# Performance work log

Measured on AMD Instinct MI355X. Metric: run time of the kernel, lower is better.

## Reference

```python
import jax, jax.numpy as jnp
import numpy as np

N = 50000      # nodes
E = 800000     # edges (before self-loops)
H = 4          # attention heads
C = 32         # out_features per head
DIN = 128      # in_features (== H*C so residual path is active)
ED = 16        # edge_dim
NEG = 0.2      # LeakyReLU negative slope (GATConv default)
EPS = 1e-5     # LayerNorm eps


def setup_inputs() -> dict:
    key = jax.random.key(0)
    ks = jax.random.split(key, 12)
    s = 0.05
    return {
        "x": jax.random.normal(ks[0], (N, DIN), dtype=jnp.float32),
        "edge_index": jax.random.randint(ks[1], (2, E), 0, N, dtype=jnp.int64),
        "edge_attr": jax.random.normal(ks[2], (E, ED), dtype=jnp.float32),
        # edge_processor: Linear(ED, ED) + ReLU (dropout = identity at eval)
        "W_ep": jax.random.normal(ks[3], (ED, ED), dtype=jnp.float32) * s,
        "b_ep": jnp.zeros((ED,), dtype=jnp.float32),
        # GATConv params (lin / lin_edge are bias-free in PyG)
        "W_lin": jax.random.normal(ks[4], (DIN, H * C), dtype=jnp.float32) * s,
        "W_edge": jax.random.normal(ks[5], (ED, H * C), dtype=jnp.float32) * s,
        "att_src": jax.random.normal(ks[6], (H, C), dtype=jnp.float32) * s,
        "att_dst": jax.random.normal(ks[7], (H, C), dtype=jnp.float32) * s,
        "att_edge": jax.random.normal(ks[8], (H, C), dtype=jnp.float32) * s,
        "bias": jnp.zeros((H * C,), dtype=jnp.float32),
        # LayerNorm params
        "ln_g": jnp.ones((H * C,), dtype=jnp.float32),
        "ln_b": jnp.zeros((H * C,), dtype=jnp.float32),
    }


def reference(x, edge_index, edge_attr, W_ep, b_ep, W_lin, W_edge,
              att_src, att_dst, att_edge, bias, ln_g, ln_b):
    n = x.shape[0]
    src, dst = edge_index[0], edge_index[1]

    # edge_processor: Linear + ReLU
    ea = jax.nn.relu(edge_attr @ W_ep + b_ep)                       # [E, ED]

    # add self-loops (PyG GATConv default), loop edge_attr = mean of incoming
    ones = jnp.ones((ea.shape[0],), dtype=ea.dtype)
    deg = jax.ops.segment_sum(ones, dst, num_segments=n)            # [N]
    loop_attr = jax.ops.segment_sum(ea, dst, num_segments=n)
    loop_attr = loop_attr / jnp.maximum(deg, 1.0)[:, None]          # [N, ED]
    loop = jnp.arange(n, dtype=src.dtype)
    src2 = jnp.concatenate([src, loop])                             # [E+N]
    dst2 = jnp.concatenate([dst, loop])
    ea2 = jnp.concatenate([ea, loop_attr], axis=0)                  # [E+N, ED]

    # node / edge linear transforms
    h = (x @ W_lin).reshape(n, H, C)                                # [N, H, C]
    a_src = jnp.einsum('nhc,hc->nh', h, att_src)                    # [N, H]
    a_dst = jnp.einsum('nhc,hc->nh', h, att_dst)
    e = (ea2 @ W_edge).reshape(-1, H, C)                            # [E+N, H, C]
    a_e = jnp.einsum('ehc,hc->eh', e, att_edge)                     # [E+N, H]

    # per-edge attention logits + leaky relu
    alpha = a_src[src2] + a_dst[dst2] + a_e                         # [E+N, H]
    alpha = jnp.where(alpha >= 0, alpha, NEG * alpha)

    # segment softmax over incoming edges of each dst node
    m = jax.ops.segment_max(alpha, dst2, num_segments=n)            # [N, H]
    ex = jnp.exp(alpha - m[dst2])
    denom = jax.ops.segment_sum(ex, dst2, num_segments=n)           # [N, H]
    w = ex / denom[dst2]                                            # [E+N, H]

    # scatter-aggregate messages
    msg = h[src2] * w[:, :, None]                                   # [E+N, H, C]
    out = jax.ops.segment_sum(msg, dst2, num_segments=n)            # [N, H, C]
    out = out.reshape(n, H * C) + bias

    # residual (DIN == H*C) + LayerNorm
    out = out + x
    mu = jnp.mean(out, axis=-1, keepdims=True)
    var = jnp.var(out, axis=-1, keepdims=True)
    out = (out - mu) * jax.lax.rsqrt(var + EPS) * ln_g + ln_b
    return out
```

## Files before the change

### kernel.cpp

```cpp
#include <hip/hip_runtime.h>
#include <hip/hip_fp16.h>
#include <math.h>

#define NN   50000
#define EE   800000
#define HH   4
#define CC   32
#define DINN 128
#define ED   16
#define NEGS 0.2f
#define LNEPS 1e-5f
#define SCAN_NB ((NN + 255) / 256)

struct __align__(16) Rec {
    float4  expa;
    __half2 ae01;
    __half2 ae23;
    int     src;
    int     pad;
};

struct __align__(8) Hp { __half2 a, b; };

__global__ __launch_bounds__(256, 2) void k_node(
        const float* __restrict__ x, const float* __restrict__ W_lin,
        const float* __restrict__ att_src, const float* __restrict__ att_dst,
        __half* __restrict__ hb, float* __restrict__ a_src, float* __restrict__ a_dst) {
    __shared__ float Wl[DINN * DINN];
    __shared__ float xr[32 * DINN];
    int t = threadIdx.x;

    {
        const float4* Wg = (const float4*)W_lin;
        float4* Ws = (float4*)Wl;
        #pragma unroll
        for (int i = 0; i < 16; ++i) Ws[t + 256 * i] = Wg[t + 256 * i];
    }
    int row0 = blockIdx.x * 32;
    {
        const float4* xg = (const float4*)x;
        float4* xs = (float4*)xr;
        #pragma unroll
        for (int i = 0; i < 4; ++i) {
            int idx = t + 256 * i;
            int row = row0 + (idx >> 5);
            float4 v = make_float4(0.f, 0.f, 0.f, 0.f);
            if (row < NN) v = xg[(long)row * 32 + (idx & 31)];
            xs[idx] = v;
        }
    }
    __syncthreads();

    int cg = t & 31, rg = t >> 5;
    int j0 = cg * 4;
    float acc[4][4] = {};
    #pragma unroll 4
    for (int k = 0; k < DINN; ++k) {
        float4 w = *(const float4*)&Wl[k * DINN + j0];
        #pragma unroll
        for (int i = 0; i < 4; ++i) {
            float xv = xr[(rg * 4 + i) * DINN + k];
            acc[i][0] = fmaf(xv, w.x, acc[i][0]);
            acc[i][1] = fmaf(xv, w.y, acc[i][1]);
            acc[i][2] = fmaf(xv, w.z, acc[i][2]);
            acc[i][3] = fmaf(xv, w.w, acc[i][3]);
        }
    }

    int head = cg >> 3, c0 = (cg & 7) * 4;
    float4 as4 = *(const float4*)&att_src[head * CC + c0];
    float4 ad4 = *(const float4*)&att_dst[head * CC + c0];
    #pragma unroll
    for (int i = 0; i < 4; ++i) {
        int row = row0 + rg * 4 + i;
        if (row < NN) {
            Hp p;
            p.a = __floats2half2_rn(acc[i][0], acc[i][1]);
            p.b = __floats2half2_rn(acc[i][2], acc[i][3]);
            *(Hp*)&hb[(long)row * DINN + j0] = p;
        }
        float ps = acc[i][0] * as4.x + acc[i][1] * as4.y + acc[i][2] * as4.z + acc[i][3] * as4.w;
        float pd = acc[i][0] * ad4.x + acc[i][1] * ad4.y + acc[i][2] * ad4.z + acc[i][3] * ad4.w;
        #pragma unroll
        for (int mask = 1; mask < 8; mask <<= 1) {
            ps += __shfl_xor(ps, mask);
            pd += __shfl_xor(pd, mask);
        }
        if ((cg & 7) == 0 && row < NN) {
            a_src[row * 4 + head] = ps;
            a_dst[row * 4 + head] = pd;
        }
    }
}

__global__ __launch_bounds__(256) void k_count(const int* __restrict__ ei,
                                               int* __restrict__ cnt,
                                               int* __restrict__ rank) {
    int e = blockIdx.x * 256 + threadIdx.x;
    if (e < EE) rank[e] = atomicAdd(cnt + ei[EE + e], 1);
}

__global__ __launch_bounds__(256) void k_scanA(const int* __restrict__ cnt,
                                               int* __restrict__ partial) {
    int t = threadIdx.x, b = blockIdx.x;
    int i = b * 256 + t;
    int v = (i < NN) ? cnt[i] : 0;
    #pragma unroll
    for (int d = 1; d < 64; d <<= 1) v += __shfl_xor(v, d);
    __shared__ int wt[4];
    if ((t & 63) == 0) wt[t >> 6] = v;
    __syncthreads();
    if (t == 0) partial[b] = wt[0] + wt[1] + wt[2] + wt[3];
}

__global__ __launch_bounds__(256) void k_scanB(const int* __restrict__ partial,
                                               int* __restrict__ poff,
                                               int* __restrict__ row_start,
                                               const float* __restrict__ W_edge,
                                               const float* __restrict__ att_edge,
                                               float* __restrict__ v_edge) {
    int t = threadIdx.x;
    if (t < ED * HH) {
        int d = t >> 2, h = t & 3;
        float s = 0.f;
        for (int c = 0; c < CC; ++c)
            s += W_edge[d * (HH * CC) + h * CC + c] * att_edge[h * CC + c];
        v_edge[t] = s;
    }
    int lane = t & 63, w = t >> 6;
    int v = (t < SCAN_NB) ? partial[t] : 0;
    int sv = v;
    #pragma unroll
    for (int d = 1; d < 64; d <<= 1) {
        int o = __shfl_up(sv, d);
        if (lane >= d) sv += o;
    }
    __shared__ int wt[4];
    if (lane == 63) wt[w] = sv;
    __syncthreads();
    int base = 0;
    for (int j = 0; j < w; ++j) base += wt[j];
    if (t < SCAN_NB) poff[t] = base + sv - v;
    if (t == 255) row_start[NN] = wt[0] + wt[1] + wt[2] + wt[3];
}

__global__ __launch_bounds__(256) void k_scanC(const int* __restrict__ cnt,
                                               const int* __restrict__ poff,
                                               int* __restrict__ row_start) {
    int t = threadIdx.x, b = blockIdx.x;
    int i = b * 256 + t;
    int v = (i < NN) ? cnt[i] : 0;
    int lane = t & 63, w = t >> 6;
    int sv = v;
    #pragma unroll
    for (int d = 1; d < 64; d <<= 1) {
        int o = __shfl_up(sv, d);
        if (lane >= d) sv += o;
    }
    __shared__ int wt[4];
    if (lane == 63) wt[w] = sv;
    __syncthreads();
    int base = 0;
    for (int j = 0; j < w; ++j) base += wt[j];
    if (i < NN) row_start[i] = poff[b] + base + sv - v;
}

__global__ __launch_bounds__(256) void k_edge2(
        const int* __restrict__ ei, const float* __restrict__ edge_attr,
        const float* __restrict__ W_ep, const float* __restrict__ b_ep,
        const float* __restrict__ v_edge,
        const float* __restrict__ a_src, const float* __restrict__ a_dst,
        const int* __restrict__ row_start, const int* __restrict__ rank,
        Rec* __restrict__ rec) {
    __shared__ float Wl[ED * ED];
    __shared__ float bl[ED];
    __shared__ float vl[ED * 4];
    int t = threadIdx.x;
    if (t < ED * ED) Wl[t] = W_ep[t];
    if (t < ED) bl[t] = b_ep[t];
    if (t < ED * 4) vl[t] = v_edge[t];
    __syncthreads();

    int e = blockIdx.x * 256 + t;
    if (e >= EE) return;

    float a[ED];
    const float4* ap = (const float4*)(edge_attr + (long)e * ED);
    float4 a0 = ap[0], a1 = ap[1], a2 = ap[2], a3 = ap[3];
    a[0]=a0.x; a[1]=a0.y; a[2]=a0.z; a[3]=a0.w;
    a[4]=a1.x; a[5]=a1.y; a[6]=a1.z; a[7]=a1.w;
    a[8]=a2.x; a[9]=a2.y; a[10]=a2.z; a[11]=a2.w;
    a[12]=a3.x; a[13]=a3.y; a[14]=a3.z; a[15]=a3.w;

    float r[ED];
    #pragma unroll
    for (int j = 0; j < ED; ++j) r[j] = bl[j];
    #pragma unroll
    for (int d = 0; d < ED; ++d) {
        float av = a[d];
        #pragma unroll
        for (int j = 0; j < ED; ++j) r[j] = fmaf(av, Wl[d * ED + j], r[j]);
    }

    float ae0 = 0.f, ae1 = 0.f, ae2 = 0.f, ae3 = 0.f;
    #pragma unroll
    for (int d = 0; d < ED; ++d) {
        float rd = fmaxf(r[d], 0.f);
        ae0 = fmaf(rd, vl[d * 4 + 0], ae0);
        ae1 = fmaf(rd, vl[d * 4 + 1], ae1);
        ae2 = fmaf(rd, vl[d * 4 + 2], ae2);
        ae3 = fmaf(rd, vl[d * 4 + 3], ae3);
    }

    int src = ei[e];
    int dst = ei[EE + e];
    float4 s4 = *(const float4*)&a_src[src * 4];
    float4 d4 = *(const float4*)&a_dst[dst * 4];
    float v0 = s4.x + d4.x + ae0;
    float v1 = s4.y + d4.y + ae1;
    float v2 = s4.z + d4.z + ae2;
    float v3 = s4.w + d4.w + ae3;
    v0 = (v0 >= 0.f) ? v0 : NEGS * v0;
    v1 = (v1 >= 0.f) ? v1 : NEGS * v1;
    v2 = (v2 >= 0.f) ? v2 : NEGS * v2;
    v3 = (v3 >= 0.f) ? v3 : NEGS * v3;

    Rec rc;
    rc.expa = make_float4(__expf(v0), __expf(v1), __expf(v2), __expf(v3));
    rc.ae01 = __floats2half2_rn(ae0, ae1);
    rc.ae23 = __floats2half2_rn(ae2, ae3);
    rc.src  = src;
    rc.pad  = 0;
    rec[row_start[dst] + rank[e]] = rc;
}

__global__ __launch_bounds__(256) void k_aggregate(
        const float* __restrict__ x, const __half2* __restrict__ hb,
        const float* __restrict__ a_src, const float* __restrict__ a_dst,
        const int* __restrict__ row_start, const Rec* __restrict__ rec,
        const float* __restrict__ bias, const float* __restrict__ ln_g,
        const float* __restrict__ ln_b, float* __restrict__ out) {
    int t = threadIdx.x;
    int wave = t >> 6, lane = t & 63;
    int n = blockIdx.x * 4 + wave;
    if (n >= NN) return;

    int start = row_start[n];
    int deg   = row_start[n + 1] - start;

    bool h1 = (lane & 32) != 0;
    bool h0 = (lane & 16) != 0;
    float accx = 0.f, accy = 0.f, s_own = 0.f, aes_own = 0.f;

    auto doEdge = [&](const Rec& r, __half2 hv) {
        float4 e4 = r.expa;
        float2 ef = h1 ? make_float2(e4.z, e4.w) : make_float2(e4.x, e4.y);
        float w = h0 ? ef.y : ef.x;
        float2 aef = __half22float2(h1 ? r.ae23 : r.ae01);
        aes_own += h0 ? aef.y : aef.x;
        s_own += w;
        float2 hf = __half22float2(hv);
        accx = fmaf(w, hf.x, accx);
        accy = fmaf(w, hf.y, accy);
    };

    const Rec* rp = rec + start;
    int k = 0;
    for (; k + 4 <= deg; k += 4) {
        Rec r0 = rp[k], r1 = rp[k + 1], r2 = rp[k + 2], r3 = rp[k + 3];
        __half2 v0 = hb[(long)r0.src * 64 + lane];
        __half2 v1 = hb[(long)r1.src * 64 + lane];
        __half2 v2 = hb[(long)r2.src * 64 + lane];
        __half2 v3 = hb[(long)r3.src * 64 + lane];
        doEdge(r0, v0); doEdge(r1, v1); doEdge(r2, v2); doEdge(r3, v3);
    }
    for (; k < deg; ++k) {
        Rec r = rp[k];
        doEdge(r, hb[(long)r.src * 64 + lane]);
    }

    int head = lane >> 4;
    float inv_deg = 1.0f / fmaxf((float)deg, 1.0f);
    float v = a_src[n * 4 + head] + a_dst[n * 4 + head] + aes_own * inv_deg;
    v = (v >= 0.f) ? v : NEGS * v;
    float w0 = __expf(v);
    s_own += w0;
    float2 hn = __half22float2(hb[(long)n * 64 + lane]);
    accx = fmaf(w0, hn.x, accx);
    accy = fmaf(w0, hn.y, accy);
    float is = 1.0f / s_own;
    accx *= is; accy *= is;

    int c0 = lane * 2;
    float2 b2 = *(const float2*)&bias[c0];
    float2 x2 = *(const float2*)&x[(long)n * DINN + c0];
    float oa = accx + b2.x + x2.x;
    float ob = accy + b2.y + x2.y;
    float sum = oa + ob, sumsq = oa * oa + ob * ob;
    #pragma unroll
    for (int d2 = 1; d2 < 64; d2 <<= 1) {
        sum   += __shfl_xor(sum, d2);
        sumsq += __shfl_xor(sumsq, d2);
    }
    float mu  = sum * (1.0f / DINN);
    float var = sumsq * (1.0f / DINN) - mu * mu;
    float rs  = rsqrtf(var + LNEPS);
    float2 g2  = *(const float2*)&ln_g[c0];
    float2 lb2 = *(const float2*)&ln_b[c0];
    float2 o2;
    o2.x = (oa - mu) * rs * g2.x + lb2.x;
    o2.y = (ob - mu) * rs * g2.y + lb2.y;
    *(float2*)&out[(long)n * DINN + c0] = o2;
}

extern "C" void kernel_launch(void* const* d_in, const int* in_sizes, int n_in,
                              void* d_out, int out_size, void* d_ws, size_t ws_size,
                              hipStream_t stream) {
    const float* x         = (const float*)d_in[0];
    const int*   ei        = (const int*)d_in[1];
    const float* edge_attr = (const float*)d_in[2];
    const float* W_ep      = (const float*)d_in[3];
    const float* b_ep      = (const float*)d_in[4];
    const float* W_lin     = (const float*)d_in[5];
    const float* W_edge    = (const float*)d_in[6];
    const float* att_src   = (const float*)d_in[7];
    const float* att_dst   = (const float*)d_in[8];
    const float* att_edge  = (const float*)d_in[9];
    const float* bias      = (const float*)d_in[10];
    const float* ln_g      = (const float*)d_in[11];
    const float* ln_b      = (const float*)d_in[12];
    float* out = (float*)d_out;

    char* ws = (char*)d_ws;
    size_t o = 0;
    auto take = [&](size_t bytes) -> char* {
        char* p = ws + o;
        o = (o + bytes + 255) & ~(size_t)255;
        return p;
    };
    __half* hbuf      = (__half*)take((size_t)NN * DINN * 2);
    float*  a_src     = (float*)take((size_t)NN * 4 * 4);
    float*  a_dst     = (float*)take((size_t)NN * 4 * 4);
    float*  v_edge    = (float*)take((size_t)ED * 4 * 4);
    int*    cnt       = (int*)  take((size_t)NN * 4);
    int*    row_start = (int*)  take((size_t)(NN + 1) * 4);
    int*    rank      = (int*)  take((size_t)EE * 4);
    int*    partial   = (int*)  take((size_t)SCAN_NB * 4);
    int*    poff      = (int*)  take((size_t)SCAN_NB * 4);
    Rec*    rec       = (Rec*)  take((size_t)EE * sizeof(Rec));

    hipMemsetAsync(cnt, 0, (size_t)NN * 4, stream);

    k_node<<<(NN + 31) / 32, 256, 0, stream>>>(x, W_lin, att_src, att_dst,
                                               hbuf, a_src, a_dst);
    k_count<<<(EE + 255) / 256, 256, 0, stream>>>(ei, cnt, rank);
    k_scanA<<<SCAN_NB, 256, 0, stream>>>(cnt, partial);
    k_scanB<<<1, 256, 0, stream>>>(partial, poff, row_start, W_edge, att_edge, v_edge);
    k_scanC<<<SCAN_NB, 256, 0, stream>>>(cnt, poff, row_start);
    k_edge2<<<(EE + 255) / 256, 256, 0, stream>>>(ei, edge_attr, W_ep, b_ep, v_edge,
                                                  a_src, a_dst, row_start, rank, rec);
    k_aggregate<<<(NN + 3) / 4, 256, 0, stream>>>(x, (const __half2*)hbuf,
                                                  a_src, a_dst, row_start, rec,
                                                  bias, ln_g, ln_b, out);
}
```

Measured before the change: 305.5 us.

## Split edge records into packed half2 weights plus separate CSR source array

The per-edge record changes from a 32-byte struct (fp32 exp weights, half attention terms, src) to a 16-byte packed array of half2 (exp, edge logit) per head plus a separate int source array. The aggregation kernel reads only its head's 4-byte word and batches 8 edges per iteration so more gathers are in flight. The node projection kernel no longer stages W_lin in LDS: it reads it from global/cache, uses 64-row tiles with a padded x tile and an 8-column register block per thread, and raises occupancy to 3 blocks per SM. Storing exp weights in half precision adds rounding and overflow risk for large logits.

```diff
diff --git a/kernel.cpp b/kernel.cpp
--- a/kernel.cpp
+++ b/kernel.cpp
@@ -12,81 +12,84 @@
 #define LNEPS 1e-5f
 #define SCAN_NB ((NN + 255) / 256)
 
-struct __align__(16) Rec {
-    float4  expa;
-    __half2 ae01;
-    __half2 ae23;
-    int     src;
-    int     pad;
-};
-
-struct __align__(8) Hp { __half2 a, b; };
-
-__global__ __launch_bounds__(256, 2) void k_node(
+struct __align__(16) Hp4 { __half2 a, b, c, d; };
+
+__global__ __launch_bounds__(256, 3) void k_node(
         const float* __restrict__ x, const float* __restrict__ W_lin,
         const float* __restrict__ att_src, const float* __restrict__ att_dst,
         __half* __restrict__ hb, float* __restrict__ a_src, float* __restrict__ a_dst) {
-    __shared__ float Wl[DINN * DINN];
-    __shared__ float xr[32 * DINN];
+    __shared__ float xr[64 * 132];
     int t = threadIdx.x;
-
-    {
-        const float4* Wg = (const float4*)W_lin;
-        float4* Ws = (float4*)Wl;
-        #pragma unroll
-        for (int i = 0; i < 16; ++i) Ws[t + 256 * i] = Wg[t + 256 * i];
-    }
-    int row0 = blockIdx.x * 32;
-    {
-        const float4* xg = (const float4*)x;
-        float4* xs = (float4*)xr;
+    int row0 = blockIdx.x * 64;
+
+    #pragma unroll
+    for (int i = 0; i < 8; ++i) {
+        int idx = t + 256 * i;
+        int r = idx >> 5, kq = idx & 31;
+        int row = row0 + r;
+        float4 v = make_float4(0.f, 0.f, 0.f, 0.f);
+        if (row < NN) v = ((const float4*)x)[(long)row * 32 + kq];
+        *(float4*)&xr[r * 132 + kq * 4] = v;
+    }
+    __syncthreads();
+
+    int colg = t & 15, rowg = t >> 4;
+    int c0 = colg * 8;
+    const float* Wp = W_lin + c0;
+    float acc[4][8] = {};
+
+    #pragma unroll 2
+    for (int k = 0; k < DINN; k += 2) {
+        float4 wa0 = *(const float4*)&Wp[(long)k * DINN];
+        float4 wb0 = *(const float4*)&Wp[(long)k * DINN + 4];
+        float4 wa1 = *(const float4*)&Wp[(long)(k + 1) * DINN];
+        float4 wb1 = *(const float4*)&Wp[(long)(k + 1) * DINN + 4];
         #pragma unroll
         for (int i = 0; i < 4; ++i) {
-            int idx = t + 256 * i;
-            int row = row0 + (idx >> 5);
-            float4 v = make_float4(0.f, 0.f, 0.f, 0.f);
-            if (row < NN) v = xg[(long)row * 32 + (idx & 31)];
-            xs[idx] = v;
-        }
-    }
-    __syncthreads();
-
-    int cg = t & 31, rg = t >> 5;
-    int j0 = cg * 4;
-    float acc[4][4] = {};
-    #pragma unroll 4
-    for (int k = 0; k < DINN; ++k) {
-        float4 w = *(const float4*)&Wl[k * DINN + j0];
-        #pragma unroll
-        for (int i = 0; i < 4; ++i) {
-            float xv = xr[(rg * 4 + i) * DINN + k];
-            acc[i][0] = fmaf(xv, w.x, acc[i][0]);
-            acc[i][1] = fmaf(xv, w.y, acc[i][1]);
-            acc[i][2] = fmaf(xv, w.z, acc[i][2]);
-            acc[i][3] = fmaf(xv, w.w, acc[i][3]);
-        }
-    }
-
-    int head = cg >> 3, c0 = (cg & 7) * 4;
-    float4 as4 = *(const float4*)&att_src[head * CC + c0];
-    float4 ad4 = *(const float4*)&att_dst[head * CC + c0];
+            float2 xv = *(const float2*)&xr[(rowg * 4 + i) * 132 + k];
+            acc[i][0] = fmaf(xv.x, wa0.x, acc[i][0]);
+            acc[i][1] = fmaf(xv.x, wa0.y, acc[i][1]);
+            acc[i][2] = fmaf(xv.x, wa0.z, acc[i][2]);
+            acc[i][3] = fmaf(xv.x, wa0.w, acc[i][3]);
+            acc[i][4] = fmaf(xv.x, wb0.x, acc[i][4]);
+            acc[i][5] = fmaf(xv.x, wb0.y, acc[i][5]);
+            acc[i][6] = fmaf(xv.x, wb0.z, acc[i][6]);
+            acc[i][7] = fmaf(xv.x, wb0.w, acc[i][7]);
+            acc[i][0] = fmaf(xv.y, wa1.x, acc[i][0]);
+            acc[i][1] = fmaf(xv.y, wa1.y, acc[i][1]);
+            acc[i][2] = fmaf(xv.y, wa1.z, acc[i][2]);
+            acc[i][3] = fmaf(xv.y, wa1.w, acc[i][3]);
+            acc[i][4] = fmaf(xv.y, wb1.x, acc[i][4]);
+            acc[i][5] = fmaf(xv.y, wb1.y, acc[i][5]);
+            acc[i][6] = fmaf(xv.y, wb1.z, acc[i][6]);
+            acc[i][7] = fmaf(xv.y, wb1.w, acc[i][7]);
+        }
+    }
+
+    int head = colg >> 2;
+    int cw = c0 & 31;
+    float4 as0 = *(const float4*)&att_src[head * CC + cw];
+    float4 as1 = *(const float4*)&att_src[head * CC + cw + 4];
+    float4 ad0 = *(const float4*)&att_dst[head * CC + cw];
+    float4 ad1 = *(const float4*)&att_dst[head * CC + cw + 4];
     #pragma unroll
     for (int i = 0; i < 4; ++i) {
-        int row = row0 + rg * 4 + i;
+        int row = row0 + rowg * 4 + i;
         if (row < NN) {
-            Hp p;
+            Hp4 p;
             p.a = __floats2half2_rn(acc[i][0], acc[i][1]);
             p.b = __floats2half2_rn(acc[i][2], acc[i][3]);
-            *(Hp*)&hb[(long)row * DINN + j0] = p;
-        }
-        float ps = acc[i][0] * as4.x + acc[i][1] * as4.y + acc[i][2] * as4.z + acc[i][3] * as4.w;
-        float pd = acc[i][0] * ad4.x + acc[i][1] * ad4.y + acc[i][2] * ad4.z + acc[i][3] * ad4.w;
-        #pragma unroll
-        for (int mask = 1; mask < 8; mask <<= 1) {
-            ps += __shfl_xor(ps, mask);
-            pd += __shfl_xor(pd, mask);
-        }
-        if ((cg & 7) == 0 && row < NN) {
+            p.c = __floats2half2_rn(acc[i][4], acc[i][5]);
+            p.d = __floats2half2_rn(acc[i][6], acc[i][7]);
+            *(Hp4*)&hb[(long)row * DINN + c0] = p;
+        }
+        float ps = acc[i][0]*as0.x + acc[i][1]*as0.y + acc[i][2]*as0.z + acc[i][3]*as0.w
+                 + acc[i][4]*as1.x + acc[i][5]*as1.y + acc[i][6]*as1.z + acc[i][7]*as1.w;
+        float pd = acc[i][0]*ad0.x + acc[i][1]*ad0.y + acc[i][2]*ad0.z + acc[i][3]*ad0.w
+                 + acc[i][4]*ad1.x + acc[i][5]*ad1.y + acc[i][6]*ad1.z + acc[i][7]*ad1.w;
+        ps += __shfl_xor(ps, 1); ps += __shfl_xor(ps, 2);
+        pd += __shfl_xor(pd, 1); pd += __shfl_xor(pd, 2);
+        if ((colg & 3) == 0 && row < NN) {
             a_src[row * 4 + head] = ps;
             a_dst[row * 4 + head] = pd;
         }
@@ -171,7 +174,7 @@
         const float* __restrict__ v_edge,
         const float* __restrict__ a_src, const float* __restrict__ a_dst,
         const int* __restrict__ row_start, const int* __restrict__ rank,
-        Rec* __restrict__ rec) {
+        uint4* __restrict__ pk, int* __restrict__ csr_src) {
     __shared__ float Wl[ED * ED];
     __shared__ float bl[ED];
     __shared__ float vl[ED * 4];
@@ -225,19 +228,21 @@
     v2 = (v2 >= 0.f) ? v2 : NEGS * v2;
     v3 = (v3 >= 0.f) ? v3 : NEGS * v3;
 
-    Rec rc;
-    rc.expa = make_float4(__expf(v0), __expf(v1), __expf(v2), __expf(v3));
-    rc.ae01 = __floats2half2_rn(ae0, ae1);
-    rc.ae23 = __floats2half2_rn(ae2, ae3);
-    rc.src  = src;
-    rc.pad  = 0;
-    rec[row_start[dst] + rank[e]] = rc;
+    __half2 p0 = __floats2half2_rn(__expf(v0), ae0);
+    __half2 p1 = __floats2half2_rn(__expf(v1), ae1);
+    __half2 p2 = __floats2half2_rn(__expf(v2), ae2);
+    __half2 p3 = __floats2half2_rn(__expf(v3), ae3);
+    int pos = row_start[dst] + rank[e];
+    pk[pos] = make_uint4(*(unsigned*)&p0, *(unsigned*)&p1,
+                         *(unsigned*)&p2, *(unsigned*)&p3);
+    csr_src[pos] = src;
 }
 
 __global__ __launch_bounds__(256) void k_aggregate(
         const float* __restrict__ x, const __half2* __restrict__ hb,
         const float* __restrict__ a_src, const float* __restrict__ a_dst,
-        const int* __restrict__ row_start, const Rec* __restrict__ rec,
+        const int* __restrict__ row_start,
+        const unsigned* __restrict__ pkh, const int* __restrict__ srcs,
         const float* __restrict__ bias, const float* __restrict__ ln_g,
         const float* __restrict__ ln_b, float* __restrict__ out) {
     int t = threadIdx.x;
@@ -247,39 +252,45 @@
 
     int start = row_start[n];
     int deg   = row_start[n + 1] - start;
-
-    bool h1 = (lane & 32) != 0;
-    bool h0 = (lane & 16) != 0;
+    int head  = lane >> 4;
+
     float accx = 0.f, accy = 0.f, s_own = 0.f, aes_own = 0.f;
-
-    auto doEdge = [&](const Rec& r, __half2 hv) {
-        float4 e4 = r.expa;
-        float2 ef = h1 ? make_float2(e4.z, e4.w) : make_float2(e4.x, e4.y);
-        float w = h0 ? ef.y : ef.x;
-        float2 aef = __half22float2(h1 ? r.ae23 : r.ae01);
-        aes_own += h0 ? aef.y : aef.x;
-        s_own += w;
+    const unsigned* pp = pkh + (size_t)start * 4 + head;
+    const int* sp = srcs + start;
+
+    int k = 0;
+    for (; k + 8 <= deg; k += 8) {
+        unsigned pv[8]; int sv[8];
+        #pragma unroll
+        for (int j = 0; j < 8; ++j) {
+            pv[j] = pp[(size_t)(k + j) * 4];
+            sv[j] = sp[k + j];
+        }
+        __half2 hv[8];
+        #pragma unroll
+        for (int j = 0; j < 8; ++j) hv[j] = hb[(long)sv[j] * 64 + lane];
+        #pragma unroll
+        for (int j = 0; j < 8; ++j) {
+            float2 wf = __half22float2(*(__half2*)&pv[j]);
+            s_own += wf.x;
+            aes_own += wf.y;
+            float2 hf = __half22float2(hv[j]);
+            accx = fmaf(wf.x, hf.x, accx);
+            accy = fmaf(wf.x, hf.y, accy);
+        }
+    }
+    for (; k < deg; ++k) {
+        unsigned p = pp[(size_t)k * 4];
+        int src = sp[k];
+        __half2 hv = hb[(long)src * 64 + lane];
+        float2 wf = __half22float2(*(__half2*)&p);
+        s_own += wf.x;
+        aes_own += wf.y;
         float2 hf = __half22float2(hv);
-        accx = fmaf(w, hf.x, accx);
-        accy = fmaf(w, hf.y, accy);
-    };
-
-    const Rec* rp = rec + start;
-    int k = 0;
-    for (; k + 4 <= deg; k += 4) {
-        Rec r0 = rp[k], r1 = rp[k + 1], r2 = rp[k + 2], r3 = rp[k + 3];
-        __half2 v0 = hb[(long)r0.src * 64 + lane];
-        __half2 v1 = hb[(long)r1.src * 64 + lane];
-        __half2 v2 = hb[(long)r2.src * 64 + lane];
-        __half2 v3 = hb[(long)r3.src * 64 + lane];
-        doEdge(r0, v0); doEdge(r1, v1); doEdge(r2, v2); doEdge(r3, v3);
-    }
-    for (; k < deg; ++k) {
-        Rec r = rp[k];
-        doEdge(r, hb[(long)r.src * 64 + lane]);
-    }
-
-    int head = lane >> 4;
+        accx = fmaf(wf.x, hf.x, accx);
+        accy = fmaf(wf.x, hf.y, accy);
+    }
+
     float inv_deg = 1.0f / fmaxf((float)deg, 1.0f);
     float v = a_src[n * 4 + head] + a_dst[n * 4 + head] + aes_own * inv_deg;
     v = (v >= 0.f) ? v : NEGS * v;
@@ -347,19 +358,22 @@
     int*    rank      = (int*)  take((size_t)EE * 4);
     int*    partial   = (int*)  take((size_t)SCAN_NB * 4);
     int*    poff      = (int*)  take((size_t)SCAN_NB * 4);
-    Rec*    rec       = (Rec*)  take((size_t)EE * sizeof(Rec));
+    uint4*  pk        = (uint4*)take((size_t)EE * 16);
+    int*    csr_src   = (int*)  take((size_t)EE * 4);
 
     hipMemsetAsync(cnt, 0, (size_t)NN * 4, stream);
 
-    k_node<<<(NN + 31) / 32, 256, 0, stream>>>(x, W_lin, att_src, att_dst,
+    k_node<<<(NN + 63) / 64, 256, 0, stream>>>(x, W_lin, att_src, att_dst,
                                                hbuf, a_src, a_dst);
     k_count<<<(EE + 255) / 256, 256, 0, stream>>>(ei, cnt, rank);
     k_scanA<<<SCAN_NB, 256, 0, stream>>>(cnt, partial);
     k_scanB<<<1, 256, 0, stream>>>(partial, poff, row_start, W_edge, att_edge, v_edge);
     k_scanC<<<SCAN_NB, 256, 0, stream>>>(cnt, poff, row_start);
     k_edge2<<<(EE + 255) / 256, 256, 0, stream>>>(ei, edge_attr, W_ep, b_ep, v_edge,
-                                                  a_src, a_dst, row_start, rank, rec);
+                                                  a_src, a_dst, row_start, rank,
+                                                  pk, csr_src);
     k_aggregate<<<(NN + 3) / 4, 256, 0, stream>>>(x, (const __half2*)hbuf,
-                                                  a_src, a_dst, row_start, rec,
+                                                  a_src, a_dst, row_start,
+                                                  (const unsigned*)pk, csr_src,
                                                   bias, ln_g, ln_b, out);
 }
```

After: 293.8 us. -3.8%, faster.
